# Kernel optimization log

Hardware: AMD Instinct MI355X
Metric: run time of the kernel (lower is better)

The kernel has to match this reference:

```python
import jax, jax.numpy as jnp
import numpy as np

EMBED_DIM = 1024
HEAD_DIM = 64


def setup_inputs() -> dict:
    key = jax.random.key(0)
    ks = jax.random.split(key, 7)
    s_in = EMBED_DIM ** -0.5  # torch Linear default init scale
    x = jax.random.normal(ks[0], (4, 4096, EMBED_DIM), dtype=jnp.float32)
    Wk = jax.random.uniform(ks[1], (HEAD_DIM, EMBED_DIM), jnp.float32, -s_in, s_in)
    bk = jax.random.uniform(ks[2], (HEAD_DIM,), jnp.float32, -s_in, s_in)
    Wq = jax.random.uniform(ks[3], (HEAD_DIM, EMBED_DIM), jnp.float32, -s_in, s_in)
    bq = jax.random.uniform(ks[4], (HEAD_DIM,), jnp.float32, -s_in, s_in)
    Wv = jax.random.uniform(ks[5], (HEAD_DIM, EMBED_DIM), jnp.float32, -s_in, s_in)
    bv = jax.random.uniform(ks[6], (HEAD_DIM,), jnp.float32, -s_in, s_in)
    return {"x": x, "Wq": Wq, "bq": bq, "Wk": Wk, "bk": bk, "Wv": Wv, "bv": bv}


def reference(x, Wq, bq, Wk, bk, Wv, bv):
    # torch Linear: y = x @ W.T + b
    q = jnp.einsum('btc,dc->btd', x, Wq) + bq  # [B,T,D]
    k = jnp.einsum('btc,dc->btd', x, Wk) + bk
    v = jnp.einsum('btc,dc->btd', x, Wv) + bv
    scale = HEAD_DIM ** -0.5
    # NOTE: original divides by scale (multiplies by sqrt(head_dim)) -- faithful
    scores = jnp.einsum('btd,bsd->bts', q, k) / scale  # [B,T,T]
    attn_weights = jax.nn.softmax(scores, axis=-1)
    return jnp.einsum('bts,bsd->btd', attn_weights, v)
```

## Files before the change

kernel.cpp:

```cpp
#include <hip/hip_runtime.h>

#define BATCH 4
#define SEQ   4096
#define CDIM  1024
#define DDIM  64
#define NROW  (BATCH * SEQ)
#define NSPL  8
#define SEG   (NROW * DDIM)

typedef _Float16 f16;
typedef _Float16 f16x8 __attribute__((ext_vector_type(8)));
typedef _Float16 f16x4 __attribute__((ext_vector_type(4)));
typedef __fp16   h16x2 __attribute__((ext_vector_type(2)));
typedef float    f32x4 __attribute__((ext_vector_type(4)));

#define MFMA32(a, b, c) __builtin_amdgcn_mfma_f32_16x16x32_f16((a), (b), (c), 0, 0, 0)
#define MFMA16(a, b, c) __builtin_amdgcn_mfma_f32_16x16x16f16((a), (b), (c), 0, 0, 0)

#define GLDS(g, l)                                                            \
  __builtin_amdgcn_global_load_lds((const __attribute__((address_space(1))) void*)(g), \
                                   (__attribute__((address_space(3))) void*)(l), 16, 0, 0)

#define QSCALE 11.5415603f

__device__ inline f16x8 cvt8(f32x4 a, f32x4 b) {
  h16x2 p0 = __builtin_amdgcn_cvt_pkrtz(a[0], a[1]);
  h16x2 p1 = __builtin_amdgcn_cvt_pkrtz(a[2], a[3]);
  h16x2 p2 = __builtin_amdgcn_cvt_pkrtz(b[0], b[1]);
  h16x2 p3 = __builtin_amdgcn_cvt_pkrtz(b[2], b[3]);
  f16x8 r;
  r[0] = p0[0]; r[1] = p0[1]; r[2] = p1[0]; r[3] = p1[1];
  r[4] = p2[0]; r[5] = p2[1]; r[6] = p3[0]; r[7] = p3[1];
  return r;
}

__device__ inline f16x4 cvt4(float a, float b, float c, float d) {
  h16x2 lo = __builtin_amdgcn_cvt_pkrtz(a, b);
  h16x2 hi = __builtin_amdgcn_cvt_pkrtz(c, d);
  f16x4 r;
  r[0] = lo[0]; r[1] = lo[1]; r[2] = hi[0]; r[3] = hi[1];
  return r;
}

__global__ __launch_bounds__(256) void prep_w_kernel(const float* __restrict__ Wq,
                                                     const float* __restrict__ Wk,
                                                     const float* __restrict__ Wv,
                                                     f16* __restrict__ wf2) {
  const int t = blockIdx.x * 256 + threadIdx.x;
  const int lane = t & 63;
  const int s = t >> 6;
  const int mt = s >> 5, ck = s & 31;
  const int mat = mt >> 2, tile = mt & 3;
  const int n = lane & 15, quad = lane >> 4;
  const float* W = (mat == 0) ? Wq : (mat == 1) ? Wk : Wv;
  const float* src = W + (size_t)(tile * 16 + n) * CDIM + ck * 32 + quad * 8;
  const f32x4 a = *(const f32x4*)src;
  const f32x4 b = *(const f32x4*)(src + 4);
  *(f16x8*)(wf2 + (size_t)t * 8) = cvt8(a, b);
}

__global__ __launch_bounds__(256, 4) void proj_kernel(const float* __restrict__ x,
                                                      const f16* __restrict__ wf2,
                                                      const float* __restrict__ bq,
                                                      const float* __restrict__ bk,
                                                      const float* __restrict__ bv,
                                                      f16* __restrict__ qs,
                                                      f16* __restrict__ ks,
                                                      f16* __restrict__ vc) {
  __shared__ __attribute__((aligned(16))) char lx[3 * 8192];
  const int tid = threadIdx.x, lane = tid & 63, w = tid >> 6;
  const int n = lane & 15, quad = lane >> 4;
  const int rowbase = blockIdx.x * 16;
  const int mtb = 3 * w;

  const float* xsrc[2];
#pragma unroll
  for (int j = 0; j < 2; ++j) {
    const int id = 2 * w + j;
    const int r = id * 2 + (lane >> 5);
    const int c = (lane & 31) ^ r;
    xsrc[j] = x + (size_t)(rowbase + r) * CDIM + c * 4;
  }

  auto issue = [&](int ck, int bufi) {
    char* base = &lx[bufi * 8192];
#pragma unroll
    for (int j = 0; j < 2; ++j)
      GLDS(xsrc[j] + ck * 128, base + (2 * w + j) * 1024);
  };

  const f16* wl = wf2 + (size_t)mtb * 16384 + lane * 8;

  f32x4 acc[3];
#pragma unroll
  for (int i = 0; i < 3; ++i) acc[i] = (f32x4){0.f, 0.f, 0.f, 0.f};

  issue(0, 0);
  issue(1, 1);
  for (int ck = 0; ck < 8; ++ck) {
    const int bufi = ck % 3;
    if (ck + 2 < 8) issue(ck + 2, (ck + 2) % 3);
    if (ck + 2 < 8)      asm volatile("s_waitcnt vmcnt(4)" ::: "memory");
    else if (ck + 1 < 8) asm volatile("s_waitcnt vmcnt(2)" ::: "memory");
    else                 asm volatile("s_waitcnt vmcnt(0)" ::: "memory");
    __builtin_amdgcn_s_barrier();
    __builtin_amdgcn_sched_barrier(0);
    const char* xb = &lx[bufi * 8192] + n * 512;
#pragma unroll
    for (int kk = 0; kk < 4; ++kk) {
      const int c1 = kk * 8 + quad * 2;
      const f32x4 xa = *(const f32x4*)(xb + ((c1 ^ n) << 4));
      const f32x4 xc = *(const f32x4*)(xb + (((c1 + 1) ^ n) << 4));
      const f16x8 af = cvt8(xa, xc);
      const f16* wq = wl + (size_t)(ck * 4 + kk) * 512;
      const f16x8 w0 = *(const f16x8*)(wq);
      const f16x8 w1 = *(const f16x8*)(wq + 16384);
      const f16x8 w2 = *(const f16x8*)(wq + 32768);
      acc[0] = MFMA32(af, w0, acc[0]);
      acc[1] = MFMA32(af, w1, acc[1]);
      acc[2] = MFMA32(af, w2, acc[2]);
    }
    __builtin_amdgcn_s_barrier();
  }

  const int r0 = rowbase + quad * 4;
#pragma unroll
  for (int i2 = 0; i2 < 3; ++i2) {
    const int mt = mtb + i2;
    const int mat = mt >> 2, tile = mt & 3;
    const int d = tile * 16 + n;
    const f32x4 aa = acc[i2];
    if (mat == 0) {
      const float bi = bq[d];
#pragma unroll
      for (int r = 0; r < 4; ++r)
        qs[(size_t)(r0 + r) * DDIM + d] = (f16)((aa[r] + bi) * QSCALE);
    } else if (mat == 1) {
      const float bi = bk[d];
#pragma unroll
      for (int r = 0; r < 4; ++r) {
        const int tt = r0 + r;
        const int col = ((((d >> 3) ^ (tt & 7)) << 3) | (d & 7));
        ks[(size_t)tt * DDIM + col] = (f16)(aa[r] + bi);
      }
    } else {
      const float bi = bv[d];
      const int bb = r0 >> 12;
      const int tl = r0 & (SEQ - 1);
      const int ck2 = tl >> 6;
      const int bsw = (((tl & 63) >> 2) ^ n) << 2;
      *(f16x4*)(vc + ((size_t)(bb * 64 + ck2) * 64 + d) * 64 + bsw) =
          cvt4(aa[0] + bi, aa[1] + bi, aa[2] + bi, aa[3] + bi);
    }
  }
}

template <int NSPLIT>
__global__ __launch_bounds__(256, 3) void attn_kernel(const f16* __restrict__ qs,
                                                      const f16* __restrict__ ks,
                                                      const f16* __restrict__ vc,
                                                      float* __restrict__ outp,
                                                      f16* __restrict__ pacc,
                                                      float* __restrict__ pm,
                                                      float* __restrict__ pl) {
  __shared__ __attribute__((aligned(16))) f16 lk[3 * 4096];
  __shared__ __attribute__((aligned(16))) f16 lv[3 * 4096];
  const int tid = threadIdx.x, lane = tid & 63, w = tid >> 6;
  const int n = lane & 15, quad = lane >> 4;
  const int split = blockIdx.x % NSPLIT;
  const int rowblk = blockIdx.x / NSPLIT;
  const int row0 = rowblk * 128 + w * 32;
  const int bb = row0 >> 12;
  const int kbase = split * (SEQ / NSPLIT);
  const int kc0 = kbase >> 6;
  const int NC = SEQ / NSPLIT / 64;

  const f16* ksb = ks + (size_t)bb * SEQ * DDIM;
  const f16* vcb = vc + (size_t)bb * 64 * 4096;

  auto issue = [&](int c, int bufi) {
#pragma unroll
    for (int i = 0; i < 2; ++i) {
      const int id = 2 * w + i;
      GLDS(ksb + (size_t)(kbase + c * 64) * 64 + id * 512 + lane * 8,
           &lk[bufi * 4096 + id * 512]);
      GLDS(vcb + (size_t)(kc0 + c) * 4096 + id * 512 + lane * 8,
           &lv[bufi * 4096 + id * 512]);
    }
  };

  f16x8 qf[2][2];
#pragma unroll
  for (int g = 0; g < 2; ++g)
#pragma unroll
    for (int hh = 0; hh < 2; ++hh)
      qf[g][hh] = *(const f16x8*)(qs + (size_t)(row0 + g * 16 + n) * DDIM + hh * 32 + quad * 8);

  const int kswz = (quad ^ (n & 7)) << 3;
  int vswz[4];
#pragma unroll
  for (int st = 0; st < 4; ++st) vswz[st] = ((((st << 2) | quad) ^ n) << 2);

  f32x4 acc[2][4];
  float m[2] = {-1e30f, -1e30f}, ll[2] = {0.f, 0.f};
#pragma unroll
  for (int g = 0; g < 2; ++g)
#pragma unroll
    for (int t = 0; t < 4; ++t) acc[g][t] = (f32x4){0.f, 0.f, 0.f, 0.f};

  issue(0, 0);
  issue(1, 1);
  for (int c = 0; c < NC; ++c) {
    const int bufi = c % 3;
    if (c + 2 < NC) issue(c + 2, (c + 2) % 3);
    if (c + 2 < NC)      asm volatile("s_waitcnt vmcnt(8)" ::: "memory");
    else if (c + 1 < NC) asm volatile("s_waitcnt vmcnt(4)" ::: "memory");
    else                 asm volatile("s_waitcnt vmcnt(0)" ::: "memory");
    __builtin_amdgcn_s_barrier();
    __builtin_amdgcn_sched_barrier(0);

    f32x4 s[2][4];
#pragma unroll
    for (int st = 0; st < 4; ++st) {
      const f16* lkr = &lk[bufi * 4096 + (st * 16 + n) * 64];
      const f16x8 klo = *(const f16x8*)(lkr + kswz);
      const f16x8 khi = *(const f16x8*)(lkr + (kswz ^ 32));
#pragma unroll
      for (int g = 0; g < 2; ++g) {
        f32x4 z = (f32x4){0.f, 0.f, 0.f, 0.f};
        z = MFMA32(klo, qf[g][0], z);
        s[g][st] = MFMA32(khi, qf[g][1], z);
      }
    }

    f16x4 pq[2][4];
#pragma unroll
    for (int g = 0; g < 2; ++g) {
      f32x4 mx;
#pragma unroll
      for (int r = 0; r < 4; ++r)
        mx[r] = fmaxf(fmaxf(s[g][0][r], s[g][1][r]), fmaxf(s[g][2][r], s[g][3][r]));
      float mloc = fmaxf(fmaxf(mx[0], mx[1]), fmaxf(mx[2], mx[3]));
      mloc = fmaxf(mloc, __shfl_xor(mloc, 16));
      mloc = fmaxf(mloc, __shfl_xor(mloc, 32));
      const float mnew = fmaxf(m[g], mloc);
      const float alpha = __builtin_amdgcn_exp2f(m[g] - mnew);
      m[g] = mnew;
      float psum = 0.f;
#pragma unroll
      for (int st = 0; st < 4; ++st) {
        f32x4 p;
#pragma unroll
        for (int r = 0; r < 4; ++r) p[r] = __builtin_amdgcn_exp2f(s[g][st][r] - mnew);
        psum += (p[0] + p[1]) + (p[2] + p[3]);
        pq[g][st] = cvt4(p[0], p[1], p[2], p[3]);
      }
      ll[g] = ll[g] * alpha + psum;
#pragma unroll
      for (int t = 0; t < 4; ++t) acc[g][t] *= alpha;
    }

#pragma unroll
    for (int dt = 0; dt < 4; ++dt) {
      const f16* lvr = &lv[bufi * 4096 + (dt * 16 + n) * 64];
#pragma unroll
      for (int st = 0; st < 4; ++st) {
        const f16x4 va = *(const f16x4*)(lvr + vswz[st]);
        acc[0][dt] = MFMA16(va, pq[0][st], acc[0][dt]);
        acc[1][dt] = MFMA16(va, pq[1][st], acc[1][dt]);
      }
    }
    __builtin_amdgcn_s_barrier();
  }

  float lred[2];
#pragma unroll
  for (int g = 0; g < 2; ++g) {
    float l = ll[g];
    l += __shfl_xor(l, 16);
    l += __shfl_xor(l, 32);
    lred[g] = l;
  }

  if (NSPLIT == 1) {
#pragma unroll
    for (int g = 0; g < 2; ++g) {
      const float inv = 1.0f / lred[g];
      const int q = row0 + g * 16 + n;
#pragma unroll
      for (int t = 0; t < 4; ++t) {
        f32x4 o = acc[g][t];
#pragma unroll
        for (int r = 0; r < 4; ++r) o[r] *= inv;
        *(f32x4*)(outp + (size_t)q * DDIM + t * 16 + quad * 4) = o;
      }
    }
  } else {
#pragma unroll
    for (int g = 0; g < 2; ++g) {
      const int q0 = row0 + g * 16;
      f16* pb = pacc + (size_t)split * SEG + ((size_t)q0 << 6) + n * 16 + quad * 4;
#pragma unroll
      for (int t = 0; t < 4; ++t)
        *(f16x4*)(pb + t * 256) =
            cvt4(acc[g][t][0], acc[g][t][1], acc[g][t][2], acc[g][t][3]);
      if (quad == 0) {
        pm[split * NROW + q0 + n] = m[g];
        pl[split * NROW + q0 + n] = lred[g];
      }
    }
  }
}

template <int NSPLIT>
__global__ __launch_bounds__(256) void combine_kernel(const f16* __restrict__ pacc,
                                                      const float* __restrict__ pm,
                                                      const float* __restrict__ pl,
                                                      float* __restrict__ out) {
  const int idx = blockIdx.x * 256 + threadIdx.x;
  const int row = idx >> 4;
  const int c = (idx & 15) * 4;
  const size_t off = ((size_t)(row & ~15) << 6) + ((size_t)(c >> 4) << 8) +
                     ((row & 15) << 4) + (c & 15);
  float mm = pm[row];
#pragma unroll
  for (int s = 1; s < NSPLIT; ++s) mm = fmaxf(mm, pm[s * NROW + row]);
  float L = 0.f;
  f32x4 o = (f32x4){0.f, 0.f, 0.f, 0.f};
#pragma unroll
  for (int s = 0; s < NSPLIT; ++s) {
    const float e = __builtin_amdgcn_exp2f(pm[s * NROW + row] - mm);
    L += pl[s * NROW + row] * e;
    const f16x4 a = *(const f16x4*)(pacc + (size_t)s * SEG + off);
#pragma unroll
    for (int j = 0; j < 4; ++j) o[j] += (float)a[j] * e;
  }
  const float inv = 1.0f / L;
#pragma unroll
  for (int j = 0; j < 4; ++j) o[j] *= inv;
  *(f32x4*)(out + (size_t)row * DDIM + c) = o;
}

extern "C" void kernel_launch(void* const* d_in, const int* in_sizes, int n_in,
                              void* d_out, int out_size, void* d_ws, size_t ws_size,
                              hipStream_t stream) {
  const float* x  = (const float*)d_in[0];
  const float* Wq = (const float*)d_in[1];
  const float* bq = (const float*)d_in[2];
  const float* Wk = (const float*)d_in[3];
  const float* bk = (const float*)d_in[4];
  const float* Wv = (const float*)d_in[5];
  const float* bv = (const float*)d_in[6];
  float* out = (float*)d_out;

  f16* wf2 = (f16*)d_ws;
  f16* qs = wf2 + 3 * 65536;
  f16* ks = qs + (size_t)SEG;
  f16* vc = ks + (size_t)SEG;
  f16* pacc = vc + (size_t)SEG;
  float* pm = (float*)(pacc + (size_t)NSPL * SEG);
  float* pl = pm + (size_t)NSPL * NROW;
  const size_t need = (size_t)((char*)(pl + (size_t)NSPL * NROW) - (char*)d_ws);

  prep_w_kernel<<<dim3(96), dim3(256), 0, stream>>>(Wq, Wk, Wv, wf2);
  proj_kernel<<<dim3(NROW / 16), dim3(256), 0, stream>>>(x, wf2, bq, bk, bv, qs, ks, vc);

  if (ws_size >= need) {
    attn_kernel<NSPL><<<dim3(128 * NSPL), dim3(256), 0, stream>>>(qs, ks, vc, nullptr, pacc, pm, pl);
    combine_kernel<NSPL><<<dim3(NROW * 16 / 256), dim3(256), 0, stream>>>(pacc, pm, pl, out);
  } else {
    attn_kernel<1><<<dim3(128), dim3(256), 0, stream>>>(qs, ks, vc, out, nullptr, nullptr, nullptr);
  }
}
```

Before: 153.1 us.

## Give each wave private LDS x buffers with deeper pipeline, drop block barriers

The projection kernel now gives each wave its own four-stage LDS ring of x chunks. Each chunk is 16 rows by 64 columns, and the rows are XOR-swizzled. Each wave loads and waits on its own data through vmcnt, so the two block-wide barriers per K step go away. In exchange, every wave fetches the same x tile again, which quadruples the global and L2 load traffic for x. LDS use rises to 64KB per block and the launch-bounds occupancy hint drops from 4 to 2.

```diff
diff --git a/kernel.cpp b/kernel.cpp
--- a/kernel.cpp
+++ b/kernel.cpp
@@ -59,7 +59,7 @@
   *(f16x8*)(wf2 + (size_t)t * 8) = cvt8(a, b);
 }
 
-__global__ __launch_bounds__(256, 4) void proj_kernel(const float* __restrict__ x,
+__global__ __launch_bounds__(256, 2) void proj_kernel(const float* __restrict__ x,
                                                       const f16* __restrict__ wf2,
                                                       const float* __restrict__ bq,
                                                       const float* __restrict__ bk,
@@ -67,26 +67,26 @@
                                                       f16* __restrict__ qs,
                                                       f16* __restrict__ ks,
                                                       f16* __restrict__ vc) {
-  __shared__ __attribute__((aligned(16))) char lx[3 * 8192];
+  __shared__ __attribute__((aligned(16))) char lx[4][4][4096];
   const int tid = threadIdx.x, lane = tid & 63, w = tid >> 6;
   const int n = lane & 15, quad = lane >> 4;
   const int rowbase = blockIdx.x * 16;
   const int mtb = 3 * w;
-
-  const float* xsrc[2];
-#pragma unroll
-  for (int j = 0; j < 2; ++j) {
-    const int id = 2 * w + j;
-    const int r = id * 2 + (lane >> 5);
-    const int c = (lane & 31) ^ r;
-    xsrc[j] = x + (size_t)(rowbase + r) * CDIM + c * 4;
-  }
-
-  auto issue = [&](int ck, int bufi) {
-    char* base = &lx[bufi * 8192];
-#pragma unroll
-    for (int j = 0; j < 2; ++j)
-      GLDS(xsrc[j] + ck * 128, base + (2 * w + j) * 1024);
+  char* lxw = &lx[w][0][0];
+
+  const float* xsrc[4];
+#pragma unroll
+  for (int j = 0; j < 4; ++j) {
+    const int r = 4 * j + (lane >> 4);
+    const int c16 = (lane & 15) ^ r;
+    xsrc[j] = x + (size_t)(rowbase + r) * CDIM + c16 * 4;
+  }
+
+  auto issue = [&](int ck, int b) {
+    char* base = lxw + b * 4096;
+#pragma unroll
+    for (int j = 0; j < 4; ++j)
+      GLDS(xsrc[j] + ck * 64, base + j * 1024 + lane * 16);
   };
 
   const f16* wl = wf2 + (size_t)mtb * 16384 + lane * 8;
@@ -97,22 +97,23 @@
 
   issue(0, 0);
   issue(1, 1);
-  for (int ck = 0; ck < 8; ++ck) {
-    const int bufi = ck % 3;
-    if (ck + 2 < 8) issue(ck + 2, (ck + 2) % 3);
-    if (ck + 2 < 8)      asm volatile("s_waitcnt vmcnt(4)" ::: "memory");
-    else if (ck + 1 < 8) asm volatile("s_waitcnt vmcnt(2)" ::: "memory");
-    else                 asm volatile("s_waitcnt vmcnt(0)" ::: "memory");
-    __builtin_amdgcn_s_barrier();
+  issue(2, 2);
+  for (int ck = 0; ck < 16; ++ck) {
+    const int b = ck & 3;
+    if (ck + 3 < 16) issue(ck + 3, (ck + 3) & 3);
+    if (ck + 3 < 16)      asm volatile("s_waitcnt vmcnt(12)" ::: "memory");
+    else if (ck + 2 < 16) asm volatile("s_waitcnt vmcnt(8)" ::: "memory");
+    else if (ck + 1 < 16) asm volatile("s_waitcnt vmcnt(4)" ::: "memory");
+    else                  asm volatile("s_waitcnt vmcnt(0)" ::: "memory");
     __builtin_amdgcn_sched_barrier(0);
-    const char* xb = &lx[bufi * 8192] + n * 512;
-#pragma unroll
-    for (int kk = 0; kk < 4; ++kk) {
-      const int c1 = kk * 8 + quad * 2;
-      const f32x4 xa = *(const f32x4*)(xb + ((c1 ^ n) << 4));
-      const f32x4 xc = *(const f32x4*)(xb + (((c1 + 1) ^ n) << 4));
+    const char* xb = lxw + b * 4096 + n * 256;
+#pragma unroll
+    for (int kk = 0; kk < 2; ++kk) {
+      const int c0 = kk * 8 + quad * 2;
+      const f32x4 xa = *(const f32x4*)(xb + ((c0 ^ n) << 4));
+      const f32x4 xc = *(const f32x4*)(xb + (((c0 + 1) ^ n) << 4));
       const f16x8 af = cvt8(xa, xc);
-      const f16* wq = wl + (size_t)(ck * 4 + kk) * 512;
+      const f16* wq = wl + (size_t)(ck * 2 + kk) * 512;
       const f16x8 w0 = *(const f16x8*)(wq);
       const f16x8 w1 = *(const f16x8*)(wq + 16384);
       const f16x8 w2 = *(const f16x8*)(wq + 32768);
@@ -120,7 +121,6 @@
       acc[1] = MFMA32(af, w1, acc[1]);
       acc[2] = MFMA32(af, w2, acc[2]);
     }
-    __builtin_amdgcn_s_barrier();
   }
 
   const int r0 = rowbase + quad * 4;
```

New measurement: 161.3 us. +5.4%, slower.

## Read K/V tiles directly from global memory instead of LDS staging

Applied to the files above, without the earlier changes.

Removes the triple-buffered LDS staging of K and V tiles (global_load_lds with waitcnt and barriers) and has each wave load its K and V fragments straight from global memory through the cache. This drops the shared-memory footprint and the per-chunk block barriers, and raises the occupancy hint in launch_bounds from 3 to 5 blocks. In exchange, the four waves of a block each fetch the same K/V data redundantly, relying on L1/L2 hits, and the explicit prefetch pipelining that hid load latency is lost.

```diff
diff --git a/kernel.cpp b/kernel.cpp
--- a/kernel.cpp
+++ b/kernel.cpp
@@ -156,15 +156,13 @@
 }
 
 template <int NSPLIT>
-__global__ __launch_bounds__(256, 3) void attn_kernel(const f16* __restrict__ qs,
+__global__ __launch_bounds__(256, 5) void attn_kernel(const f16* __restrict__ qs,
                                                       const f16* __restrict__ ks,
                                                       const f16* __restrict__ vc,
                                                       float* __restrict__ outp,
                                                       f16* __restrict__ pacc,
                                                       float* __restrict__ pm,
                                                       float* __restrict__ pl) {
-  __shared__ __attribute__((aligned(16))) f16 lk[3 * 4096];
-  __shared__ __attribute__((aligned(16))) f16 lv[3 * 4096];
   const int tid = threadIdx.x, lane = tid & 63, w = tid >> 6;
   const int n = lane & 15, quad = lane >> 4;
   const int split = blockIdx.x % NSPLIT;
@@ -178,17 +176,6 @@
   const f16* ksb = ks + (size_t)bb * SEQ * DDIM;
   const f16* vcb = vc + (size_t)bb * 64 * 4096;
 
-  auto issue = [&](int c, int bufi) {
-#pragma unroll
-    for (int i = 0; i < 2; ++i) {
-      const int id = 2 * w + i;
-      GLDS(ksb + (size_t)(kbase + c * 64) * 64 + id * 512 + lane * 8,
-           &lk[bufi * 4096 + id * 512]);
-      GLDS(vcb + (size_t)(kc0 + c) * 4096 + id * 512 + lane * 8,
-           &lv[bufi * 4096 + id * 512]);
-    }
-  };
-
   f16x8 qf[2][2];
 #pragma unroll
   for (int g = 0; g < 2; ++g)
@@ -208,23 +195,13 @@
 #pragma unroll
     for (int t = 0; t < 4; ++t) acc[g][t] = (f32x4){0.f, 0.f, 0.f, 0.f};
 
-  issue(0, 0);
-  issue(1, 1);
   for (int c = 0; c < NC; ++c) {
-    const int bufi = c % 3;
-    if (c + 2 < NC) issue(c + 2, (c + 2) % 3);
-    if (c + 2 < NC)      asm volatile("s_waitcnt vmcnt(8)" ::: "memory");
-    else if (c + 1 < NC) asm volatile("s_waitcnt vmcnt(4)" ::: "memory");
-    else                 asm volatile("s_waitcnt vmcnt(0)" ::: "memory");
-    __builtin_amdgcn_s_barrier();
-    __builtin_amdgcn_sched_barrier(0);
-
     f32x4 s[2][4];
 #pragma unroll
     for (int st = 0; st < 4; ++st) {
-      const f16* lkr = &lk[bufi * 4096 + (st * 16 + n) * 64];
-      const f16x8 klo = *(const f16x8*)(lkr + kswz);
-      const f16x8 khi = *(const f16x8*)(lkr + (kswz ^ 32));
+      const f16* kr = ksb + (size_t)(kbase + c * 64 + st * 16 + n) * 64;
+      const f16x8 klo = *(const f16x8*)(kr + kswz);
+      const f16x8 khi = *(const f16x8*)(kr + (kswz ^ 32));
 #pragma unroll
       for (int g = 0; g < 2; ++g) {
         f32x4 z = (f32x4){0.f, 0.f, 0.f, 0.f};
@@ -260,17 +237,17 @@
       for (int t = 0; t < 4; ++t) acc[g][t] *= alpha;
     }
 
+    const f16* vt = vcb + (size_t)(kc0 + c) * 4096;
 #pragma unroll
     for (int dt = 0; dt < 4; ++dt) {
-      const f16* lvr = &lv[bufi * 4096 + (dt * 16 + n) * 64];
+      const f16* vr = vt + (dt * 16 + n) * 64;
 #pragma unroll
       for (int st = 0; st < 4; ++st) {
-        const f16x4 va = *(const f16x4*)(lvr + vswz[st]);
+        const f16x4 va = *(const f16x4*)(vr + vswz[st]);
         acc[0][dt] = MFMA16(va, pq[0][st], acc[0][dt]);
         acc[1][dt] = MFMA16(va, pq[1][st], acc[1][dt]);
       }
     }
-    __builtin_amdgcn_s_barrier();
   }
 
   float lred[2];
```

After: 204.3 us. 33.5% more time.
